# Kernel optimization log

Hardware: AMD Instinct MI355X
Metric: run time of the kernel (lower is better)

Reference implementation:

```python
import jax, jax.numpy as jnp
import numpy as np

EPS = 1e-5

def layer_norm(x, gamma, beta):
    # biased variance (unbiased=False), matching torch code
    mean = jnp.mean(x, axis=-1, keepdims=True)
    var = jnp.mean((x - mean) ** 2, axis=-1, keepdims=True)
    return (x - mean) / jnp.sqrt(var + EPS) * gamma + beta

def setup_inputs() -> dict:
    key = jax.random.key(0)
    ks = jax.random.split(key, 8)
    B, T, C, H = 2, 2048, 768, 12
    Dff = 4 * C
    s = lambda n: 1.0 / np.sqrt(n)
    return {
        "x": jax.random.normal(ks[0], (B, T, C), dtype=jnp.float32),
        "mask": jnp.ones((B, T), dtype=jnp.int32),
        "Wqkv": jax.random.normal(ks[1], (C, 3 * C), dtype=jnp.float32) * s(C),
        "bqkv": jnp.zeros((3 * C,), dtype=jnp.float32),
        "Wp": jax.random.normal(ks[2], (C, C), dtype=jnp.float32) * s(C),
        "bp": jnp.zeros((C,), dtype=jnp.float32),
        "gamma1": jnp.ones((1, 1, C), dtype=jnp.float32),
        "beta1": jnp.zeros((1, 1, C), dtype=jnp.float32),
        "W1": jax.random.normal(ks[3], (C, Dff), dtype=jnp.float32) * s(C),
        "b1": jnp.zeros((Dff,), dtype=jnp.float32),
        "W2": jax.random.normal(ks[4], (Dff, C), dtype=jnp.float32) * s(Dff),
        "b2": jnp.zeros((C,), dtype=jnp.float32),
        "gamma2": jnp.ones((1, 1, C), dtype=jnp.float32),
        "beta2": jnp.zeros((1, 1, C), dtype=jnp.float32),
    }

def reference(x, mask, Wqkv, bqkv, Wp, bp, gamma1, beta1, W1, b1, W2, b2, gamma2, beta2):
    B, T, C = x.shape
    H = 12
    D = C // H
    # --- multi-head attention (hand-rolled QK^T-softmax-V) ---
    qkv = x @ Wqkv + bqkv                                  # (B,T,3C)
    q, k, v = jnp.split(qkv, 3, axis=-1)
    q = q.reshape(B, T, H, D).transpose(0, 2, 1, 3)        # (B,H,T,D)
    k = k.reshape(B, T, H, D).transpose(0, 2, 1, 3)
    v = v.reshape(B, T, H, D).transpose(0, 2, 1, 3)
    scores = jnp.einsum('bhtd,bhsd->bhts', q, k) * (D ** -0.5)  # (B,H,T,T)
    pad = (mask == 0)[:, None, None, :]                    # (B,1,1,T)
    scores = jnp.where(pad, -jnp.inf, scores)
    weights = jax.nn.softmax(scores, axis=-1)
    attn = jnp.einsum('bhts,bhsd->bhtd', weights, v)       # (B,H,T,D)
    attn = attn.transpose(0, 2, 1, 3).reshape(B, T, C)
    attn = attn @ Wp + bp
    # --- post-sublayer LN then residual (as in source) ---
    out = x + layer_norm(attn, gamma1, beta1)
    # --- MLP with exact GELU ---
    h = jax.nn.gelu(out @ W1 + b1, approximate=False)
    mlp = h @ W2 + b2
    out = out + layer_norm(mlp, gamma2, beta2)
    return out
```

## Files before the change

### kernel.cpp

```cpp
#include <hip/hip_runtime.h>
#include <math.h>

#define BB 2
#define TT 2048
#define CC 768
#define NH 12
#define HD 64
#define DFF 3072
#define MM (BB*TT)

typedef _Float16 f16;
typedef unsigned long long u64;
typedef unsigned int u32;
typedef __attribute__((ext_vector_type(8))) _Float16 f16x8;
typedef __attribute__((ext_vector_type(4))) _Float16 f16x4;
typedef __attribute__((ext_vector_type(4))) float f32x4;
typedef __attribute__((ext_vector_type(2))) unsigned int u32x2;
typedef __attribute__((ext_vector_type(4))) unsigned int u32x4;

#define QSCALE 0.18033688011112042f

#define GLD_LDS(gptr, lptr) \
  __builtin_amdgcn_global_load_lds((const __attribute__((address_space(1))) void*)(gptr), \
                                   (__attribute__((address_space(3))) void*)(lptr), 16, 0, 0)

#if __has_builtin(__builtin_amdgcn_exp2f)
#define EXP2(x) __builtin_amdgcn_exp2f(x)
#else
#define EXP2(x) exp2f(x)
#endif

#if __has_builtin(__builtin_amdgcn_rcpf)
#define RCP(x) __builtin_amdgcn_rcpf(x)
#else
#define RCP(x) (1.f / (x))
#endif

#if __has_builtin(__builtin_amdgcn_permlane32_swap) && __has_builtin(__builtin_amdgcn_permlane16_swap)
#define HAVE_PERMLANE_SWAP 1
#else
#define HAVE_PERMLANE_SWAP 0
#endif

__device__ __forceinline__ u32 pkrtz(float a, float b)
{
    auto h = __builtin_amdgcn_cvt_pkrtz(a, b);
    return __builtin_bit_cast(u32, h);
}

__device__ __forceinline__ float gelu_f(float x)
{
    const float y = fabsf(x) * 0.70710678118654752f;
    const float t = RCP(fmaf(0.3275911f, y, 1.f));
    float p = fmaf(1.061405429f, t, -1.453152027f);
    p = fmaf(p, t, 1.421413741f);
    p = fmaf(p, t, -0.284496736f);
    p = fmaf(p, t, 0.254829592f);
    p = p * t;
    const float e = EXP2(-y * y * 1.4426950408889634f);
    const float er = copysignf(1.f - p * e, x);
    return 0.5f * x * (1.f + er);
}

__device__ __forceinline__ void transpose_tile(const float* __restrict__ W,
                                               f16* __restrict__ Wt,
                                               int K, int N, int idx,
                                               float tile[32][33])
{
    const int kx = idx % (K / 32), ny = idx / (K / 32);
    const int k0 = kx * 32, n0 = ny * 32;
    const int r  = threadIdx.x >> 3;
    const int c4 = (threadIdx.x & 7) * 4;
    float4 v = *(const float4*)&W[(size_t)(k0 + r) * N + n0 + c4];
    tile[r][c4 + 0] = v.x; tile[r][c4 + 1] = v.y;
    tile[r][c4 + 2] = v.z; tile[r][c4 + 3] = v.w;
    __syncthreads();
    f16x4 o = {(f16)tile[c4 + 0][r], (f16)tile[c4 + 1][r],
               (f16)tile[c4 + 2][r], (f16)tile[c4 + 3][r]};
    *(f16x4*)&Wt[(size_t)(n0 + r) * K + k0 + c4] = o;
}

__global__ __launch_bounds__(256)
void conv_all(const float* __restrict__ x, f16* __restrict__ xh,
              const float* __restrict__ Wqkv, f16* __restrict__ Wqkvt,
              const float* __restrict__ Wp, f16* __restrict__ Wpt,
              const float* __restrict__ W1, f16* __restrict__ W1t,
              const float* __restrict__ W2, f16* __restrict__ W2t)
{
    __shared__ float tile[32][33];
    const int blk = blockIdx.x;
    if (blk < 3072) {
        const int i = blk * 256 + threadIdx.x;
        float4 v = ((const float4*)x)[i];
        f16x4 o = {(f16)v.x, (f16)v.y, (f16)v.z, (f16)v.w};
        ((f16x4*)xh)[i] = o;
    } else if (blk < 4800) {
        transpose_tile(Wqkv, Wqkvt, CC, 3 * CC, blk - 3072, tile);
    } else if (blk < 5376) {
        transpose_tile(Wp, Wpt, CC, CC, blk - 4800, tile);
    } else if (blk < 7680) {
        transpose_tile(W1, W1t, CC, DFF, blk - 5376, tile);
    } else {
        transpose_tile(W2, W2t, DFF, CC, blk - 7680, tile);
    }
}

template<int TM, int OUT_MODE, int GELU, int SPLITK, int AMODE>
__global__ __launch_bounds__(256)
void gemm_mfma(const f16* __restrict__ A, const f16* __restrict__ Bt,
               const float* __restrict__ bias, void* __restrict__ Cout,
               f16* __restrict__ Kout, f16* __restrict__ Vout,
               const int* __restrict__ maskp, int M, int N, int K,
               const f16* __restrict__ Ao1,
               const float* __restrict__ lp0, const float* __restrict__ lp1)
{
    constexpr int NT = (TM == 128) ? 4 : 2;
    constexpr int G  = 512 / TM;
    __shared__ f16 As[2][TM * 32];
    __shared__ f16 Bs[2][128 * 32];

    int id = blockIdx.x;
    int kk = 0;
    if (SPLITK == 2) { kk = id & 1; id >>= 1; }
    const int xcd = id & 7, j = id >> 3;
    const int by = xcd * G + (j & (G - 1));
    const int bx = j / G;
    const int Keff = K / SPLITK;

    const int t = threadIdx.x;
    const int lane = t & 63, w = t >> 6;
    const int fr = lane & 15, quad = lane >> 4;
    const int row0 = by * TM, col0 = bx * 128;
    const int wm = (TM == 128) ? (w & 1) * 64 : 0;
    const int wn = (TM == 128) ? (w >> 1) * 64 : w * 32;

    const int arow = w * (TM / 4) + (lane >> 2);
    const int brow = w * 32 + (lane >> 2);
    const int cg = (((lane & 3) ^ ((lane >> 3) & 3)) * 16);
    const char* ag = (const char*)(A  + (size_t)(row0 + arow) * K + kk * Keff) + cg;
    const char* bg = (const char*)(Bt + (size_t)(col0 + brow) * K + kk * Keff) + cg;
    const size_t rowK = (size_t)K * 2;
    const int wA = w * (TM / 4) * 32;
    const int wB = w * 32 * 32;
    const int sof = (quad ^ ((fr >> 1) & 3)) * 8;

    const f16 *a0p = nullptr, *a1p = nullptr;
    const float *lr0 = nullptr, *lr1 = nullptr;
    int lchunk8 = 0;
    f16* aswb[2] = {nullptr, nullptr};
    if (AMODE) {
        const int strow = lane >> 2, pchunk = lane & 3;
        lchunk8 = ((pchunk ^ ((lane >> 3) & 3))) * 8;
        const int ar = row0 + w * 16 + strow;
        a0p = A   + (size_t)ar * K + kk * Keff + lchunk8;
        a1p = Ao1 + (size_t)ar * K + kk * Keff + lchunk8;
        lr0 = lp0 + ar * NH;
        lr1 = lp1 + ar * NH;
        aswb[0] = &As[0][wA + strow * 32 + pchunk * 8];
        aswb[1] = &As[1][wA + strow * 32 + pchunk * 8];
    }

    f32x4 acc[4][NT] = {};

    if (AMODE) {
        f16x8 a0 = *(const f16x8*)(a0p);
        f16x8 a1 = *(const f16x8*)(a1p);
        const int hh = (kk * Keff + lchunk8) >> 6;
        const f16 lh = (f16)RCP(lr0[hh] + lr1[hh]);
        f16x8 s;
#pragma unroll
        for (int jj = 0; jj < 8; ++jj) s[jj] = (f16)((a0[jj] + a1[jj]) * lh);
        *(f16x8*)aswb[0] = s;
    } else {
        GLD_LDS(ag, &As[0][wA]);
        if (TM == 128) GLD_LDS(ag + 16 * rowK, &As[0][wA + 16 * 32]);
    }
    GLD_LDS(bg, &Bs[0][wB]);
    GLD_LDS(bg + 16 * rowK, &Bs[0][wB + 16 * 32]);

    for (int k0 = 0; k0 < Keff; k0 += 32) {
        const int buf = (k0 >> 5) & 1;
        f16x8 na0, na1; float nls = 1.f;
        if (AMODE && k0 + 32 < Keff) {
            na0 = *(const f16x8*)(a0p + k0 + 32);
            na1 = *(const f16x8*)(a1p + k0 + 32);
            const int hh = (kk * Keff + k0 + 32 + lchunk8) >> 6;
            nls = lr0[hh] + lr1[hh];
        }
        __syncthreads();
        if (k0 + 32 < Keff) {
            const size_t kb = (size_t)(k0 + 32) * 2;
            if (AMODE) {
                const f16 lh = (f16)RCP(nls);
                f16x8 s;
#pragma unroll
                for (int jj = 0; jj < 8; ++jj) s[jj] = (f16)((na0[jj] + na1[jj]) * lh);
                *(f16x8*)aswb[buf ^ 1] = s;
            } else {
                GLD_LDS(ag + kb, &As[buf ^ 1][wA]);
                if (TM == 128) GLD_LDS(ag + kb + 16 * rowK, &As[buf ^ 1][wA + 16 * 32]);
            }
            GLD_LDS(bg + kb, &Bs[buf ^ 1][wB]);
            GLD_LDS(bg + kb + 16 * rowK, &Bs[buf ^ 1][wB + 16 * 32]);
        }
        f16x8 af[4], bf[NT];
#pragma unroll
        for (int mt = 0; mt < 4; ++mt)
            af[mt] = *(const f16x8*)&As[buf][(wm + mt * 16 + fr) * 32 + sof];
#pragma unroll
        for (int nt = 0; nt < NT; ++nt)
            bf[nt] = *(const f16x8*)&Bs[buf][(wn + nt * 16 + fr) * 32 + sof];
#pragma unroll
        for (int mt = 0; mt < 4; ++mt)
#pragma unroll
            for (int nt = 0; nt < NT; ++nt)
                acc[mt][nt] = __builtin_amdgcn_mfma_f32_16x16x32_f16(
                    af[mt], bf[nt], acc[mt][nt], 0, 0, 0);
    }

    float bvs[NT];
#pragma unroll
    for (int nt = 0; nt < NT; ++nt)
        bvs[nt] = (SPLITK == 2 && kk) ? 0.f : bias[col0 + wn + nt * 16 + fr];
    f16* outbase = (f16*)Cout + (SPLITK == 2 ? (size_t)kk * M * N : 0);
#pragma unroll
    for (int mt = 0; mt < 4; ++mt) {
        const int rowb = row0 + wm + mt * 16 + quad * 4;
        float mv[4] = {1.f, 1.f, 1.f, 1.f};
        if (OUT_MODE == 2 && col0 >= 1536) {
            int4 mi = *(const int4*)&maskp[rowb];
            mv[0] = mi.x ? 1.f : 0.f; mv[1] = mi.y ? 1.f : 0.f;
            mv[2] = mi.z ? 1.f : 0.f; mv[3] = mi.w ? 1.f : 0.f;
        }
#pragma unroll
        for (int nt = 0; nt < NT; ++nt) {
            const int col = col0 + wn + nt * 16 + fr;
            if (OUT_MODE == 2) {
                const int bq = rowb >> 11, sb = rowb & 2047;
                if (col0 < 768) {
#pragma unroll
                    for (int v = 0; v < 4; ++v)
                        ((f16*)Cout)[(size_t)(rowb + v) * 768 + col]
                            = (f16)((acc[mt][nt][v] + bvs[nt]) * QSCALE);
                } else if (col0 < 1536) {
                    const int dg = col - 768;
                    const int hh = dg >> 6, dd = dg & 63;
                    f16* kb = Kout + (size_t)(bq * NH + hh) * (TT * HD);
#pragma unroll
                    for (int v = 0; v < 4; ++v) {
                        const int s = sb + v;
                        kb[((s >> 4) * 128 + (dd >> 3) * 16 + (s & 15)) * 8 + (dd & 7)]
                            = (f16)(acc[mt][nt][v] + bvs[nt]);
                    }
                } else {
                    const int dg = col - 1536;
                    const int hh = dg >> 6, dd = dg & 63;
                    f16* vb = Vout + (size_t)(bq * NH + hh) * (TT * HD);
                    f16x4 pk = {(f16)((acc[mt][nt][0] + bvs[nt]) * mv[0]),
                                (f16)((acc[mt][nt][1] + bvs[nt]) * mv[1]),
                                (f16)((acc[mt][nt][2] + bvs[nt]) * mv[2]),
                                (f16)((acc[mt][nt][3] + bvs[nt]) * mv[3])};
                    *(f16x4*)&vb[((sb >> 3) * 64 + dd) * 8 + (sb & 7)] = pk;
                }
            } else {
#pragma unroll
                for (int v = 0; v < 4; ++v) {
                    float o = acc[mt][nt][v] + bvs[nt];
                    if (GELU) o = gelu_f(o);
                    outbase[(size_t)(rowb + v) * N + col] = (f16)o;
                }
            }
        }
    }
}

__global__ __launch_bounds__(256)
void attn_mfma(const f16* __restrict__ qh, const f16* __restrict__ kth,
               const f16* __restrict__ vth, const int* __restrict__ mask,
               f16* __restrict__ O0, f16* __restrict__ O1,
               float* __restrict__ l0, float* __restrict__ l1)
{
    __shared__ __align__(16) char smem[16640];
    f16* Mf = (f16*)smem;
#if !HAVE_PERMLANE_SWAP
    f16* Ps = (f16*)(smem + 4096);
#endif
    float* Ored  = (float*)smem;
    float* lredp = (float*)(smem + 16384);

    const int id = blockIdx.x;
    const int xcd = id & 7, j = id >> 3;
    const int pair = xcd * 3 + j % 3;
    const int rem = j / 3;
    const int qt = rem >> 1, shalf = rem & 1;
    const int b = pair / NH, h = pair % NH;

    const int t = threadIdx.x, lane = t & 63, w = t >> 6;
    const int wq = w >> 1, ws = w & 1;
    const int fr = lane & 15, quad = lane >> 4;

    {
        int4 mi0 = *(const int4*)&mask[b * TT + t * 8];
        int4 mi1 = *(const int4*)&mask[b * TT + t * 8 + 4];
        f16x8 mrow;
        mrow[0] = mi0.x ? (f16)1.f : (f16)0.f; mrow[1] = mi0.y ? (f16)1.f : (f16)0.f;
        mrow[2] = mi0.z ? (f16)1.f : (f16)0.f; mrow[3] = mi0.w ? (f16)1.f : (f16)0.f;
        mrow[4] = mi1.x ? (f16)1.f : (f16)0.f; mrow[5] = mi1.y ? (f16)1.f : (f16)0.f;
        mrow[6] = mi1.z ? (f16)1.f : (f16)0.f; mrow[7] = mi1.w ? (f16)1.f : (f16)0.f;
        *(f16x8*)&Mf[t * 8] = mrow;
    }

    f16x8 qf[2][2];
#pragma unroll
    for (int nt = 0; nt < 2; ++nt)
#pragma unroll
        for (int ks = 0; ks < 2; ++ks)
            qf[nt][ks] = *(const f16x8*)&qh[(size_t)(b * TT + qt * 64 + wq * 32 + nt * 16 + fr) * CC
                                            + h * HD + ks * 32 + quad * 8];

    __syncthreads();

    const f16* KB = kth + (size_t)(b * NH + h) * (TT * HD);
    const f16* VB = vth + (size_t)(b * NH + h) * (TT * HD);
    int ko[2][2], vo[4];
#pragma unroll
    for (int mt = 0; mt < 2; ++mt)
#pragma unroll
        for (int ks = 0; ks < 2; ++ks)
            ko[mt][ks] = ((ws * 2 + mt) * 128 + (ks * 4 + quad) * 16 + fr) * 8;
#pragma unroll
    for (int nt = 0; nt < 4; ++nt)
        vo[nt] = ((ws * 4 + quad) * 64 + nt * 16 + fr) * 8;

    f32x4 oacc[2][4] = {};
    f32x4 lacc[2] = {};

    const int it0 = shalf * 16;
#pragma unroll 2
    for (int it = it0; it < it0 + 16; ++it) {
        const int ib = it * 4096;
        f16x8 vf[4];
#pragma unroll
        for (int nt = 0; nt < 4; ++nt)
            vf[nt] = *(const f16x8*)(VB + ib + vo[nt]);
        f16x8 kf[2][2];
#pragma unroll
        for (int mt = 0; mt < 2; ++mt)
#pragma unroll
            for (int ks = 0; ks < 2; ++ks)
                kf[mt][ks] = *(const f16x8*)(KB + ib + ko[mt][ks]);

        f32x4 sacc[2][2] = {};
#pragma unroll
        for (int mt = 0; mt < 2; ++mt)
#pragma unroll
            for (int nt = 0; nt < 2; ++nt) {
                sacc[mt][nt] = __builtin_amdgcn_mfma_f32_16x16x32_f16(
                    kf[mt][0], qf[nt][0], sacc[mt][nt], 0, 0, 0);
                sacc[mt][nt] = __builtin_amdgcn_mfma_f32_16x16x32_f16(
                    kf[mt][1], qf[nt][1], sacc[mt][nt], 0, 0, 0);
            }

        f16x8 mf = *(const f16x8*)&Mf[it * 64 + ws * 32 + quad * 8];

#if HAVE_PERMLANE_SWAP
#pragma unroll
        for (int nt = 0; nt < 2; ++nt) {
            const u32 pa = pkrtz(EXP2(sacc[0][nt][0]), EXP2(sacc[0][nt][1]));
            const u32 pb = pkrtz(EXP2(sacc[0][nt][2]), EXP2(sacc[0][nt][3]));
            const u32 pc = pkrtz(EXP2(sacc[1][nt][0]), EXP2(sacc[1][nt][1]));
            const u32 pd = pkrtz(EXP2(sacc[1][nt][2]), EXP2(sacc[1][nt][3]));
            const u32x2 e0 = __builtin_amdgcn_permlane32_swap(pa, pc, false, false);
            const u32x2 e1 = __builtin_amdgcn_permlane16_swap(e0.x, e0.y, false, false);
            const u32x2 e2 = __builtin_amdgcn_permlane32_swap(pb, pd, false, false);
            const u32x2 e3 = __builtin_amdgcn_permlane16_swap(e2.x, e2.y, false, false);
            const u32x4 pw = {e1.x, e3.x, e1.y, e3.y};
            const f16x8 pfr = __builtin_bit_cast(f16x8, pw);
            lacc[nt] = __builtin_amdgcn_mfma_f32_16x16x32_f16(pfr, mf, lacc[nt], 0, 0, 0);
#pragma unroll
            for (int vt = 0; vt < 4; ++vt)
                oacc[nt][vt] = __builtin_amdgcn_mfma_f32_16x16x32_f16(
                    pfr, vf[vt], oacc[nt][vt], 0, 0, 0);
        }
#else
#pragma unroll
        for (int mt = 0; mt < 2; ++mt)
#pragma unroll
            for (int nt = 0; nt < 2; ++nt) {
                f16x4 pk = {(f16)EXP2(sacc[mt][nt][0]), (f16)EXP2(sacc[mt][nt][1]),
                            (f16)EXP2(sacc[mt][nt][2]), (f16)EXP2(sacc[mt][nt][3])};
                *(f16x4*)&Ps[(wq * 32 + nt * 16 + fr) * 72 + ws * 32 + mt * 16 + quad * 4] = pk;
            }
        f16x8 pf[2];
#pragma unroll
        for (int mt = 0; mt < 2; ++mt)
            pf[mt] = *(const f16x8*)&Ps[(wq * 32 + mt * 16 + fr) * 72 + ws * 32 + quad * 8];
#pragma unroll
        for (int mt = 0; mt < 2; ++mt) {
            lacc[mt] = __builtin_amdgcn_mfma_f32_16x16x32_f16(pf[mt], mf, lacc[mt], 0, 0, 0);
#pragma unroll
            for (int nt = 0; nt < 4; ++nt)
                oacc[mt][nt] = __builtin_amdgcn_mfma_f32_16x16x32_f16(
                    pf[mt], vf[nt], oacc[mt][nt], 0, 0, 0);
        }
#endif
    }

    f16* Oout = shalf ? O1 : O0;
    float* lout = shalf ? l1 : l0;
    __syncthreads();
    if (ws == 1) {
#pragma unroll
        for (int mt = 0; mt < 2; ++mt) {
            const int q = wq * 32 + mt * 16 + quad * 4;
#pragma unroll
            for (int nt = 0; nt < 4; ++nt)
#pragma unroll
                for (int v = 0; v < 4; ++v)
                    Ored[(q + v) * 64 + nt * 16 + fr] = oacc[mt][nt][v];
            if (fr == 0)
#pragma unroll
                for (int v = 0; v < 4; ++v) lredp[q + v] = lacc[mt][v];
        }
    }
    __syncthreads();
    if (ws == 0) {
#pragma unroll
        for (int mt = 0; mt < 2; ++mt) {
            const int q0 = wq * 32 + mt * 16 + quad * 4;
            if (fr == 0)
#pragma unroll
                for (int v = 0; v < 4; ++v)
                    lout[(size_t)(b * TT + qt * 64 + q0 + v) * NH + h]
                        = lacc[mt][v] + lredp[q0 + v];
#pragma unroll
            for (int nt = 0; nt < 4; ++nt)
#pragma unroll
                for (int v = 0; v < 4; ++v) {
                    float o = oacc[mt][nt][v] + Ored[(q0 + v) * 64 + nt * 16 + fr];
                    Oout[(size_t)(b * TT + qt * 64 + q0 + v) * CC + h * HD + nt * 16 + fr]
                        = (f16)o;
                }
        }
    }
}

template<int WRITE_H>
__global__ __launch_bounds__(256)
void ln_residual(const float* __restrict__ res,
                 const f16* __restrict__ y0, const f16* __restrict__ y1,
                 const float* __restrict__ gamma, const float* __restrict__ beta,
                 float* __restrict__ outp, f16* __restrict__ outh)
{
    const int t = threadIdx.x;
    const int row = blockIdx.x * 8 + (t >> 5);
    const int c0 = (t & 31) * 24;
    const f16* yr0 = y0 + (size_t)row * CC + c0;
    const f16* yr1 = y1 + (size_t)row * CC + c0;
    float v[24];
    float s = 0.f, sq = 0.f;
#pragma unroll
    for (int i = 0; i < 3; ++i) {
        f16x8 a = *(const f16x8*)(yr0 + i * 8);
        f16x8 bb = *(const f16x8*)(yr1 + i * 8);
#pragma unroll
        for (int jj = 0; jj < 8; ++jj) {
            float vv = (float)a[jj] + (float)bb[jj];
            v[i * 8 + jj] = vv; s += vv; sq += vv * vv;
        }
    }
#pragma unroll
    for (int off = 1; off < 32; off <<= 1) {
        s  += __shfl_xor(s, off);
        sq += __shfl_xor(sq, off);
    }
    const float mean = s * (1.f / 768.f);
    const float var  = sq * (1.f / 768.f) - mean * mean;
    const float rstd = rsqrtf(var + 1e-5f);
    const float* rr = res + (size_t)row * CC + c0;
    float* orow = outp + (size_t)row * CC + c0;
#pragma unroll
    for (int i = 0; i < 6; ++i) {
        float4 r4 = *(const float4*)(rr + i * 4);
        float4 g4 = *(const float4*)(gamma + c0 + i * 4);
        float4 b4 = *(const float4*)(beta + c0 + i * 4);
        float4 o;
        o.x = r4.x + (v[i*4+0] - mean) * rstd * g4.x + b4.x;
        o.y = r4.y + (v[i*4+1] - mean) * rstd * g4.y + b4.y;
        o.z = r4.z + (v[i*4+2] - mean) * rstd * g4.z + b4.z;
        o.w = r4.w + (v[i*4+3] - mean) * rstd * g4.w + b4.w;
        *(float4*)(orow + i * 4) = o;
        if (WRITE_H) {
            f16x4 h4 = {(f16)o.x, (f16)o.y, (f16)o.z, (f16)o.w};
            *(f16x4*)(outh + (size_t)row * CC + c0 + i * 4) = h4;
        }
    }
}

extern "C" void kernel_launch(void* const* d_in, const int* in_sizes, int n_in,
                              void* d_out, int out_size, void* d_ws, size_t ws_size,
                              hipStream_t stream)
{
    const float* x     = (const float*)d_in[0];
    const int*   mask  = (const int*)  d_in[1];
    const float* Wqkv  = (const float*)d_in[2];
    const float* bqkv  = (const float*)d_in[3];
    const float* Wp    = (const float*)d_in[4];
    const float* bp    = (const float*)d_in[5];
    const float* g1    = (const float*)d_in[6];
    const float* be1   = (const float*)d_in[7];
    const float* W1    = (const float*)d_in[8];
    const float* b1    = (const float*)d_in[9];
    const float* W2    = (const float*)d_in[10];
    const float* b2    = (const float*)d_in[11];
    const float* g2    = (const float*)d_in[12];
    const float* be2   = (const float*)d_in[13];
    float* outp = (float*)d_out;

    char* wsb = (char*)d_ws;
    f16*   qhb    = (f16*)(wsb);
    f16*   kth    = (f16*)(wsb + 6291456);
    f16*   vth    = (f16*)(wsb + 12582912);
    f16*   O0     = (f16*)(wsb + 18874368);
    f16*   O1     = (f16*)(wsb + 25165824);
    f16*   hbuf   = (f16*)(wsb);
    f16*   xh     = (f16*)(wsb + 25165824);
    float* out1f  = (float*)(wsb + 25165824);
    f16*   Wqkvt  = (f16*)(wsb + 31457280);
    f16*   Wpt    = (f16*)(wsb + 34996224);
    f16*   W1t    = (f16*)(wsb + 37748736);
    f16*   W2t    = (f16*)(wsb + 42467328);
    f16*   p0     = (f16*)(wsb + 47185920);
    f16*   p1     = (f16*)(wsb + 53477376);
    f16*   out1h  = (f16*)(wsb + 59768832);
    float* l0     = (float*)(wsb + 66060288);
    float* l1     = (float*)(wsb + 66256896);

    const dim3 blk(256);

    conv_all<<<dim3(9984), blk, 0, stream>>>(x, xh, Wqkv, Wqkvt, Wp, Wpt,
                                             W1, W1t, W2, W2t);

    gemm_mfma<128, 2, 0, 1, 0><<<dim3((3 * CC / 128) * (MM / 128)), blk, 0, stream>>>(
        xh, Wqkvt, bqkv, qhb, kth, vth, mask, MM, 3 * CC, CC,
        nullptr, nullptr, nullptr);
    attn_mfma<<<dim3((TT / 64) * NH * BB * 2), blk, 0, stream>>>(
        qhb, kth, vth, mask, O0, O1, l0, l1);
    gemm_mfma<64, 1, 0, 2, 1><<<dim3(2 * (CC / 128) * (MM / 64)), blk, 0, stream>>>(
        O0, Wpt, bp, p0, nullptr, nullptr, nullptr, MM, CC, CC,
        O1, l0, l1);
    ln_residual<1><<<dim3(MM / 8), blk, 0, stream>>>(x, p0, p1, g1, be1, out1f, out1h);
    gemm_mfma<128, 1, 1, 1, 0><<<dim3((DFF / 128) * (MM / 128)), blk, 0, stream>>>(
        out1h, W1t, b1, hbuf, nullptr, nullptr, nullptr, MM, DFF, CC,
        nullptr, nullptr, nullptr);
    gemm_mfma<64, 1, 0, 2, 0><<<dim3(2 * (CC / 128) * (MM / 64)), blk, 0, stream>>>(
        hbuf, W2t, b2, p0, nullptr, nullptr, nullptr, MM, CC, DFF,
        nullptr, nullptr, nullptr);
    ln_residual<0><<<dim3(MM / 8), blk, 0, stream>>>(out1f, p0, p1, g2, be2, outp, nullptr);
}
```

Baseline: 280.0 us.

## Split attention key range into four partitions instead of two

The attention kernel now splits the key/value sequence into four quarters per query tile rather than two, which doubles the block count. Each block writes its own partial output and row-sum buffer. The projection GEMM's A-loader now sums four partial outputs and four normaliser sums before scaling. Workspace buffers are reused for the extra partials and the projection output is redirected to the freed Q buffer. The aim is more parallelism and better load balance in attention, at the cost of extra partial-output traffic and reduction work in the projection GEMM.

```diff
diff --git a/kernel.cpp b/kernel.cpp
--- a/kernel.cpp
+++ b/kernel.cpp
@@ -112,7 +112,9 @@
                f16* __restrict__ Kout, f16* __restrict__ Vout,
                const int* __restrict__ maskp, int M, int N, int K,
                const f16* __restrict__ Ao1,
-               const float* __restrict__ lp0, const float* __restrict__ lp1)
+               const float* __restrict__ lp0, const float* __restrict__ lp1,
+               const f16* __restrict__ Ao2, const f16* __restrict__ Ao3,
+               const float* __restrict__ lp2, const float* __restrict__ lp3)
 {
     constexpr int NT = (TM == 128) ? 4 : 2;
     constexpr int G  = 512 / TM;
@@ -144,8 +146,8 @@
     const int wB = w * 32 * 32;
     const int sof = (quad ^ ((fr >> 1) & 3)) * 8;
 
-    const f16 *a0p = nullptr, *a1p = nullptr;
-    const float *lr0 = nullptr, *lr1 = nullptr;
+    const f16 *a0p = nullptr, *a1p = nullptr, *a2p = nullptr, *a3p = nullptr;
+    const float *lr0 = nullptr, *lr1 = nullptr, *lr2 = nullptr, *lr3 = nullptr;
     int lchunk8 = 0;
     f16* aswb[2] = {nullptr, nullptr};
     if (AMODE) {
@@ -154,8 +156,12 @@
         const int ar = row0 + w * 16 + strow;
         a0p = A   + (size_t)ar * K + kk * Keff + lchunk8;
         a1p = Ao1 + (size_t)ar * K + kk * Keff + lchunk8;
+        a2p = Ao2 + (size_t)ar * K + kk * Keff + lchunk8;
+        a3p = Ao3 + (size_t)ar * K + kk * Keff + lchunk8;
         lr0 = lp0 + ar * NH;
         lr1 = lp1 + ar * NH;
+        lr2 = lp2 + ar * NH;
+        lr3 = lp3 + ar * NH;
         aswb[0] = &As[0][wA + strow * 32 + pchunk * 8];
         aswb[1] = &As[1][wA + strow * 32 + pchunk * 8];
     }
@@ -165,11 +171,14 @@
     if (AMODE) {
         f16x8 a0 = *(const f16x8*)(a0p);
         f16x8 a1 = *(const f16x8*)(a1p);
+        f16x8 a2 = *(const f16x8*)(a2p);
+        f16x8 a3 = *(const f16x8*)(a3p);
         const int hh = (kk * Keff + lchunk8) >> 6;
-        const f16 lh = (f16)RCP(lr0[hh] + lr1[hh]);
+        const f16 lh = (f16)RCP(lr0[hh] + lr1[hh] + lr2[hh] + lr3[hh]);
         f16x8 s;
 #pragma unroll
-        for (int jj = 0; jj < 8; ++jj) s[jj] = (f16)((a0[jj] + a1[jj]) * lh);
+        for (int jj = 0; jj < 8; ++jj)
+            s[jj] = (f16)(((a0[jj] + a1[jj]) + (a2[jj] + a3[jj])) * lh);
         *(f16x8*)aswb[0] = s;
     } else {
         GLD_LDS(ag, &As[0][wA]);
@@ -180,12 +189,14 @@
 
     for (int k0 = 0; k0 < Keff; k0 += 32) {
         const int buf = (k0 >> 5) & 1;
-        f16x8 na0, na1; float nls = 1.f;
+        f16x8 na0, na1, na2, na3; float nls = 1.f;
         if (AMODE && k0 + 32 < Keff) {
             na0 = *(const f16x8*)(a0p + k0 + 32);
             na1 = *(const f16x8*)(a1p + k0 + 32);
+            na2 = *(const f16x8*)(a2p + k0 + 32);
+            na3 = *(const f16x8*)(a3p + k0 + 32);
             const int hh = (kk * Keff + k0 + 32 + lchunk8) >> 6;
-            nls = lr0[hh] + lr1[hh];
+            nls = lr0[hh] + lr1[hh] + lr2[hh] + lr3[hh];
         }
         __syncthreads();
         if (k0 + 32 < Keff) {
@@ -194,7 +205,8 @@
                 const f16 lh = (f16)RCP(nls);
                 f16x8 s;
 #pragma unroll
-                for (int jj = 0; jj < 8; ++jj) s[jj] = (f16)((na0[jj] + na1[jj]) * lh);
+                for (int jj = 0; jj < 8; ++jj)
+                    s[jj] = (f16)(((na0[jj] + na1[jj]) + (na2[jj] + na3[jj])) * lh);
                 *(f16x8*)aswb[buf ^ 1] = s;
             } else {
                 GLD_LDS(ag + kb, &As[buf ^ 1][wA]);
@@ -278,7 +290,9 @@
 void attn_mfma(const f16* __restrict__ qh, const f16* __restrict__ kth,
                const f16* __restrict__ vth, const int* __restrict__ mask,
                f16* __restrict__ O0, f16* __restrict__ O1,
-               float* __restrict__ l0, float* __restrict__ l1)
+               f16* __restrict__ O2, f16* __restrict__ O3,
+               float* __restrict__ l0, float* __restrict__ l1,
+               float* __restrict__ l2, float* __restrict__ l3)
 {
     __shared__ __align__(16) char smem[16640];
     f16* Mf = (f16*)smem;
@@ -292,7 +306,7 @@
     const int xcd = id & 7, j = id >> 3;
     const int pair = xcd * 3 + j % 3;
     const int rem = j / 3;
-    const int qt = rem >> 1, shalf = rem & 1;
+    const int qt = rem >> 2, squat = rem & 3;
     const int b = pair / NH, h = pair % NH;
 
     const int t = threadIdx.x, lane = t & 63, w = t >> 6;
@@ -335,9 +349,9 @@
     f32x4 oacc[2][4] = {};
     f32x4 lacc[2] = {};
 
-    const int it0 = shalf * 16;
+    const int it0 = squat * 8;
 #pragma unroll 2
-    for (int it = it0; it < it0 + 16; ++it) {
+    for (int it = it0; it < it0 + 8; ++it) {
         const int ib = it * 4096;
         f16x8 vf[4];
 #pragma unroll
@@ -406,8 +420,8 @@
 #endif
     }
 
-    f16* Oout = shalf ? O1 : O0;
-    float* lout = shalf ? l1 : l0;
+    f16* Oout = (squat & 2) ? ((squat & 1) ? O3 : O2) : ((squat & 1) ? O1 : O0);
+    float* lout = (squat & 2) ? ((squat & 1) ? l3 : l2) : ((squat & 1) ? l1 : l0);
     __syncthreads();
     if (ws == 1) {
 #pragma unroll
@@ -535,6 +549,11 @@
     f16*   out1h  = (f16*)(wsb + 59768832);
     float* l0     = (float*)(wsb + 66060288);
     float* l1     = (float*)(wsb + 66256896);
+    float* l2     = (float*)(wsb + 31457280);
+    float* l3     = (float*)(wsb + 31653888);
+    f16*   O2     = p0;
+    f16*   O3     = p1;
+    f16*   pj0    = qhb;
 
     const dim3 blk(256);
 
@@ -543,18 +562,19 @@
 
     gemm_mfma<128, 2, 0, 1, 0><<<dim3((3 * CC / 128) * (MM / 128)), blk, 0, stream>>>(
         xh, Wqkvt, bqkv, qhb, kth, vth, mask, MM, 3 * CC, CC,
-        nullptr, nullptr, nullptr);
-    attn_mfma<<<dim3((TT / 64) * NH * BB * 2), blk, 0, stream>>>(
-        qhb, kth, vth, mask, O0, O1, l0, l1);
+        nullptr, nullptr, nullptr, nullptr, nullptr, nullptr, nullptr);
+    attn_mfma<<<dim3((TT / 64) * NH * BB * 4), blk, 0, stream>>>(
+        qhb, kth, vth, mask, O0, O1, O2, O3, l0, l1, l2, l3);
     gemm_mfma<64, 1, 0, 2, 1><<<dim3(2 * (CC / 128) * (MM / 64)), blk, 0, stream>>>(
-        O0, Wpt, bp, p0, nullptr, nullptr, nullptr, MM, CC, CC,
-        O1, l0, l1);
-    ln_residual<1><<<dim3(MM / 8), blk, 0, stream>>>(x, p0, p1, g1, be1, out1f, out1h);
+        O0, Wpt, bp, pj0, nullptr, nullptr, nullptr, MM, CC, CC,
+        O1, l0, l1, O2, O3, l2, l3);
+    ln_residual<1><<<dim3(MM / 8), blk, 0, stream>>>(
+        x, pj0, pj0 + (size_t)MM * CC, g1, be1, out1f, out1h);
     gemm_mfma<128, 1, 1, 1, 0><<<dim3((DFF / 128) * (MM / 128)), blk, 0, stream>>>(
         out1h, W1t, b1, hbuf, nullptr, nullptr, nullptr, MM, DFF, CC,
-        nullptr, nullptr, nullptr);
+        nullptr, nullptr, nullptr, nullptr, nullptr, nullptr, nullptr);
     gemm_mfma<64, 1, 0, 2, 0><<<dim3(2 * (CC / 128) * (MM / 64)), blk, 0, stream>>>(
         hbuf, W2t, b2, p0, nullptr, nullptr, nullptr, MM, CC, DFF,
-        nullptr, nullptr, nullptr);
+        nullptr, nullptr, nullptr, nullptr, nullptr, nullptr, nullptr);
     ln_residual<0><<<dim3(MM / 8), blk, 0, stream>>>(out1f, p0, p1, g2, be2, outp, nullptr);
 }
```

New measurement: 285.2 us. No clear change (+1.8%).
